# Performance work log

Hardware: AMD Instinct MI355X
Metric: run time of the kernel (lower is better)

## Reference

```python
import jax, jax.numpy as jnp
import numpy as np

FLOW_NUM = 2048
H = 64  # lstm_output_dim
NOISE_DIM = 3


def _w(key, shape, s=0.08):
    return (jax.random.normal(key, shape, dtype=jnp.float32) * s)


def setup_inputs() -> dict:
    key = jax.random.key(0)
    ks = jax.random.split(key, 20)
    d = {
        "noise": jax.random.normal(ks[0], (FLOW_NUM, NOISE_DIM), dtype=jnp.float32),
        "w_ih0": _w(ks[1], (4 * H, NOISE_DIM)),
        "w_hh0": _w(ks[2], (4 * H, H)),
        "b_ih0": _w(ks[3], (4 * H,)),
        "b_hh0": _w(ks[4], (4 * H,)),
        "w_ih1": _w(ks[5], (4 * H, H)),
        "w_hh1": _w(ks[6], (4 * H, H)),
        "b_ih1": _w(ks[7], (4 * H,)),
        "b_hh1": _w(ks[8], (4 * H,)),
        "w_ih2": _w(ks[9], (4 * H, H)),
        "w_hh2": _w(ks[10], (4 * H, H)),
        "b_ih2": _w(ks[11], (4 * H,)),
        "b_hh2": _w(ks[12], (4 * H,)),
        "fc1_w": _w(ks[13], (32, H)),
        "fc1_b": _w(ks[14], (32,)),
        "fc2_w": _w(ks[15], (16, 32)),
        "fc2_b": _w(ks[16], (16,)),
        "fc3_w": _w(ks[17], (3, 16)),
        "fc3_b": _w(ks[18], (3,)),
        "flow_length": 500,
    }
    return d


def _lstm_cell(x, h, c, w_ih, w_hh, b_ih, b_hh):
    # PyTorch gate order: input, forget, cell(g), output
    gates = x @ w_ih.T + h @ w_hh.T + (b_ih + b_hh)
    i, f, g, o = jnp.split(gates, 4, axis=-1)
    c_new = jax.nn.sigmoid(f) * c + jax.nn.sigmoid(i) * jnp.tanh(g)
    h_new = jax.nn.sigmoid(o) * jnp.tanh(c_new)
    return h_new, c_new


def reference(noise, w_ih0, w_hh0, b_ih0, b_hh0,
              w_ih1, w_hh1, b_ih1, b_hh1,
              w_ih2, w_hh2, b_ih2, b_hh2,
              fc1_w, fc1_b, fc2_w, fc2_b, fc3_w, fc3_b,
              flow_length):
    layers = [(w_ih0, w_hh0, b_ih0, b_hh0),
              (w_ih1, w_hh1, b_ih1, b_hh1),
              (w_ih2, w_hh2, b_ih2, b_hh2)]
    n = noise.shape[0]
    h0 = jnp.zeros((3, n, H), dtype=noise.dtype)
    c0 = jnp.zeros((3, n, H), dtype=noise.dtype)

    def step(carry, _):
        x, h, c = carry
        inp = x
        hs, cs = [], []
        for l, (wi, wh, bi, bh) in enumerate(layers):
            h_l, c_l = _lstm_cell(inp, h[l], c[l], wi, wh, bi, bh)
            hs.append(h_l)
            cs.append(c_l)
            inp = h_l
        # MLP head (Dropout is identity in eval mode); LeakyReLU slope 0.01
        y = jax.nn.leaky_relu(inp @ fc1_w.T + fc1_b)
        y = jax.nn.leaky_relu(y @ fc2_w.T + fc2_b)
        y = jax.nn.leaky_relu(y @ fc3_w.T + fc3_b)
        return (y, jnp.stack(hs), jnp.stack(cs)), y

    _, flow = jax.lax.scan(step, (noise, h0, c0), None, length=flow_length)
    # flow: [flow_length, flow_num, 3] -> [flow_num, flow_length, 3]
    return jnp.swapaxes(flow, 0, 1)
```

## Files before the change

### kernel.cpp

```cpp
#include <hip/hip_runtime.h>

#define NT 512

typedef _Float16 f16x8 __attribute__((ext_vector_type(8)));
typedef float    f32x4 __attribute__((ext_vector_type(4)));
typedef unsigned u32x4 __attribute__((ext_vector_type(4)));

#define MFMA(a, b, c) __builtin_amdgcn_mfma_f32_16x16x32_f16((a), (b), (c), 0, 0, 0)

#if __has_builtin(__builtin_amdgcn_exp2f)
__device__ __forceinline__ float fexp(float x) { return __builtin_amdgcn_exp2f(x * 1.4426950408889634f); }
#else
__device__ __forceinline__ float fexp(float x) { return __expf(x); }
#endif
#if __has_builtin(__builtin_amdgcn_rcpf)
__device__ __forceinline__ float frcp(float x) { return __builtin_amdgcn_rcpf(x); }
#else
__device__ __forceinline__ float frcp(float x) { return 1.0f / x; }
#endif
__device__ __forceinline__ float sigm(float x)  { return frcp(1.0f + fexp(-x)); }
__device__ __forceinline__ float tanh_(float x) { return 1.0f - 2.0f * frcp(1.0f + fexp(2.0f * x)); }
__device__ __forceinline__ float lrelu(float x) { return x > 0.0f ? x : 0.01f * x; }

__device__ __forceinline__ f16x8 ld8(const float* p) {
    const float4* q = (const float4*)p;
    float4 a = q[0], b = q[1];
    f16x8 r = { (_Float16)a.x, (_Float16)a.y, (_Float16)a.z, (_Float16)a.w,
                (_Float16)b.x, (_Float16)b.y, (_Float16)b.z, (_Float16)b.w };
    return r;
}

__device__ __forceinline__ unsigned pkh(float a, float b) {
    auto h = __builtin_amdgcn_cvt_pkrtz(a, b);
    return __builtin_bit_cast(unsigned, h);
}
__device__ __forceinline__ unsigned shflu(unsigned v, int lane) {
    return (unsigned)__shfl((int)v, lane, 64);
}

__global__ __launch_bounds__(NT, 2)
void gen_kernel(
    const float* __restrict__ noise,
    const float* __restrict__ w_ih0, const float* __restrict__ w_hh0,
    const float* __restrict__ b_ih0, const float* __restrict__ b_hh0,
    const float* __restrict__ w_ih1, const float* __restrict__ w_hh1,
    const float* __restrict__ b_ih1, const float* __restrict__ b_hh1,
    const float* __restrict__ w_ih2, const float* __restrict__ w_hh2,
    const float* __restrict__ b_ih2, const float* __restrict__ b_hh2,
    const float* __restrict__ fc1_w, const float* __restrict__ fc1_b,
    const float* __restrict__ fc2_w, const float* __restrict__ fc2_b,
    const float* __restrict__ fc3_w, const float* __restrict__ fc3_b,
    const int*   __restrict__ flow_len_p,
    float* __restrict__ out)
{
    __shared__ _Float16 sh[3][2][16 * 64] __attribute__((aligned(16)));
    __shared__ _Float16 sx [16][40] __attribute__((aligned(16)));
    __shared__ float so[2][8][16][3] __attribute__((aligned(16)));

    const int tid  = threadIdx.x;
    const int l    = tid & 63;
    const int w    = tid >> 6;
    const int ls   = l & 15;
    const int lj   = l >> 4;
    const int base = blockIdx.x * 8;
    const int T    = flow_len_p[0];

    const int gA  = ls & 3;
    const int rA0 = gA * 64 + 4 * (2 * w + 0) + (ls >> 2);
    const int rA1 = gA * 64 + 4 * (2 * w + 1) + (ls >> 2);

    f16x8 A1[2][4], A2[2][4], A0[2][3];
#pragma unroll
    for (int kc = 0; kc < 2; ++kc) {
        A1[0][kc]     = ld8(w_ih1 + rA0 * 64 + 32 * kc + 8 * lj);
        A1[1][kc]     = ld8(w_ih1 + rA1 * 64 + 32 * kc + 8 * lj);
        A1[0][2 + kc] = ld8(w_hh1 + rA0 * 64 + 32 * kc + 8 * lj);
        A1[1][2 + kc] = ld8(w_hh1 + rA1 * 64 + 32 * kc + 8 * lj);
        A2[0][kc]     = ld8(w_ih2 + rA0 * 64 + 32 * kc + 8 * lj);
        A2[1][kc]     = ld8(w_ih2 + rA1 * 64 + 32 * kc + 8 * lj);
        A2[0][2 + kc] = ld8(w_hh2 + rA0 * 64 + 32 * kc + 8 * lj);
        A2[1][2 + kc] = ld8(w_hh2 + rA1 * 64 + 32 * kc + 8 * lj);
        A0[0][kc]     = ld8(w_hh0 + rA0 * 64 + 32 * kc + 8 * lj);
        A0[1][kc]     = ld8(w_hh0 + rA1 * 64 + 32 * kc + 8 * lj);
    }
#pragma unroll
    for (int tt = 0; tt < 2; ++tt) {
        const int r = tt ? rA1 : rA0;
        f16x8 v;
#pragma unroll
        for (int i = 0; i < 8; ++i) {
            int kl = 8 * lj + i;
            float x = (kl < 3) ? w_ih0[r * 3 + kl]
                    : (kl == 3) ? (b_ih0[r] + b_hh0[r]) : 0.0f;
            v[i] = (_Float16)x;
        }
        A0[tt][2] = v;
    }
    f16x8 F1[2][2], F2, F3;
#pragma unroll
    for (int tt = 0; tt < 2; ++tt)
#pragma unroll
        for (int kc = 0; kc < 2; ++kc)
            F1[tt][kc] = ld8(fc1_w + (16 * tt + ls) * 64 + 32 * kc + 8 * lj);
    F2 = ld8(fc2_w + ls * 32 + 8 * lj);
    {
        f16x8 v;
#pragma unroll
        for (int i = 0; i < 8; ++i) {
            int k = 8 * lj + i;
            v[i] = (_Float16)((ls < 3 && k < 16) ? fc3_w[ls * 16 + k] : 0.0f);
        }
        F3 = v;
    }
    const int uc0 = 8 * w + lj, uc1 = 8 * w + 4 + lj;
    const int u_own = (ls < 8) ? uc0 : uc1;
    const int cs    = ls & 7;
    const int whaddr = cs * 64 + 8 * (((u_own >> 3) + cs) & 7) + (u_own & 7);
    float b1o[4], b2o[4];
#pragma unroll
    for (int g = 0; g < 4; ++g) {
        b1o[g] = b_ih1[g * 64 + u_own] + b_hh1[g * 64 + u_own];
        b2o[g] = b_ih2[g * 64 + u_own] + b_hh2[g * 64 + u_own];
    }
    float hb1a[4], hb1b[4], hb2[4];
#pragma unroll
    for (int r = 0; r < 4; ++r) {
        hb1a[r] = fc1_b[4 * lj + r];
        hb1b[r] = fc1_b[16 + 4 * lj + r];
        hb2[r]  = fc2_b[4 * lj + r];
    }
    float fb3[3] = { fc3_b[0], fc3_b[1], fc3_b[2] };

    const int s01 = ls + 16 * ((2 * lj) & 3);
    const int s23 = ls + 16 * ((2 * lj + 1) & 3);

    for (int i = tid; i < 3 * 2 * 16 * 64; i += NT) ((_Float16*)sh)[i] = (_Float16)0.0f;
    for (int i = tid; i < 16 * 40; i += NT) ((_Float16*)sx)[i] = (_Float16)0.0f;
    __syncthreads();
    if (tid < 16) sx[tid][3] = (_Float16)1.0f;
    if (tid < 24) {
        int s = tid / 3, d = tid % 3;
        sx[s][d] = (_Float16)noise[(base + s) * 3 + d];
    }

    float c0s = 0.0f, c1s = 0.0f, c2s = 0.0f;
    const float zb[4] = {0, 0, 0, 0};
    const f32x4 z4 = {0, 0, 0, 0};
    __syncthreads();

#define RD(L, p, kg) (*(const f16x8*)&sh[L][p][ls * 64 + 8 * (((kg) + ls) & 7)])

#define REPACK(cell, a0, a1)                                                   \
    float cell[4];                                                             \
    _Pragma("unroll")                                                          \
    for (int r = 0; r < 4; ++r) {                                              \
        float v_ = __shfl_xor(a1[r], 8);                                       \
        cell[r] = (ls < 8) ? a0[r] : v_;                                       \
    }

#define ACTC(cell, bo, cref, L, p) {                                           \
        float gi = cell[0] + bo[0], gf = cell[1] + bo[1];                      \
        float gg = cell[2] + bo[2], go = cell[3] + bo[3];                      \
        cref = sigm(gf) * cref + sigm(gi) * tanh_(gg);                         \
        sh[L][p][whaddr] = (_Float16)(sigm(go) * tanh_(cref)); }

    {
        f16x8 bx = *(const f16x8*)&sx[ls][8 * lj];
        f32x4 a0 = z4, a1 = z4;
        a0 = MFMA(A0[0][2], bx, a0);
        a1 = MFMA(A0[1][2], bx, a1);
        REPACK(cell, a0, a1)
        ACTC(cell, zb, c0s, 0, 0)
    }
    __syncthreads();
    f16x8 ph1a = RD(1, 1, lj), ph1b = RD(1, 1, 4 + lj);

    for (int t = 0; t < T; ++t) {
        const int pc = t & 1, pp = pc ^ 1;
        f16x8 r0 = RD(0, pc, lj), r1 = RD(0, pc, 4 + lj);
        f16x8 nh2a = RD(2, pp, lj), nh2b = RD(2, pp, 4 + lj);
        {
            f32x4 a0 = z4, a1 = z4;
            a0 = MFMA(A1[0][0], r0, a0);   a1 = MFMA(A1[1][0], r0, a1);
            a0 = MFMA(A1[0][1], r1, a0);   a1 = MFMA(A1[1][1], r1, a1);
            a0 = MFMA(A1[0][2], ph1a, a0); a1 = MFMA(A1[1][2], ph1a, a1);
            a0 = MFMA(A1[0][3], ph1b, a0); a1 = MFMA(A1[1][3], ph1b, a1);
            REPACK(cell, a0, a1)
            ACTC(cell, b1o, c1s, 1, pc)
        }
        __syncthreads();
        {
            f16x8 s0 = RD(1, pc, lj), s1 = RD(1, pc, 4 + lj);
            f32x4 a0 = z4, a1 = z4;
            a0 = MFMA(A2[0][0], s0, a0);   a1 = MFMA(A2[1][0], s0, a1);
            a0 = MFMA(A2[0][1], s1, a0);   a1 = MFMA(A2[1][1], s1, a1);
            a0 = MFMA(A2[0][2], nh2a, a0); a1 = MFMA(A2[1][2], nh2a, a1);
            a0 = MFMA(A2[0][3], nh2b, a0); a1 = MFMA(A2[1][3], nh2b, a1);
            REPACK(cell, a0, a1)
            ACTC(cell, b2o, c2s, 2, pc)
        }
        __syncthreads();
        f32x4 h0a = z4, h0b = z4;
        h0a = MFMA(A0[0][0], r0, h0a); h0b = MFMA(A0[1][0], r0, h0b);
        h0a = MFMA(A0[0][1], r1, h0a); h0b = MFMA(A0[1][1], r1, h0b);
        if (w == 0) {
            f16x8 bh0 = RD(2, pc, lj), bh1 = RD(2, pc, 4 + lj);
            f32x4 y1a = z4, y1b = z4;
            y1a = MFMA(F1[0][0], bh0, y1a); y1b = MFMA(F1[1][0], bh0, y1b);
            y1a = MFMA(F1[0][1], bh1, y1a); y1b = MFMA(F1[1][1], bh1, y1b);
            unsigned pa0 = pkh(lrelu(y1a[0] + hb1a[0]), lrelu(y1a[1] + hb1a[1]));
            unsigned pa1 = pkh(lrelu(y1a[2] + hb1a[2]), lrelu(y1a[3] + hb1a[3]));
            unsigned pb0 = pkh(lrelu(y1b[0] + hb1b[0]), lrelu(y1b[1] + hb1b[1]));
            unsigned pb1 = pkh(lrelu(y1b[2] + hb1b[2]), lrelu(y1b[3] + hb1b[3]));
            unsigned t0a = shflu(pa0, s01), t0b = shflu(pb0, s01);
            unsigned t1a = shflu(pa1, s01), t1b = shflu(pb1, s01);
            unsigned t2a = shflu(pa0, s23), t2b = shflu(pb0, s23);
            unsigned t3a = shflu(pa1, s23), t3b = shflu(pb1, s23);
            const bool lo = (lj < 2);
            u32x4 B1 = { lo ? t0a : t0b, lo ? t1a : t1b, lo ? t2a : t2b, lo ? t3a : t3b };
            f16x8 by1 = __builtin_bit_cast(f16x8, B1);
            f32x4 y2 = z4;
            y2 = MFMA(F2, by1, y2);
            unsigned q0 = pkh(lrelu(y2[0] + hb2[0]), lrelu(y2[1] + hb2[1]));
            unsigned q1 = pkh(lrelu(y2[2] + hb2[2]), lrelu(y2[3] + hb2[3]));
            unsigned z0 = shflu(q0, s01), z1 = shflu(q1, s01);
            unsigned z2 = shflu(q0, s23), z3 = shflu(q1, s23);
            u32x4 B2 = { z0, z1, z2, z3 };
            f16x8 by2 = __builtin_bit_cast(f16x8, B2);
            f32x4 y3 = z4;
            y3 = MFMA(F3, by2, y3);
            if (lj == 0) {
                float o0 = lrelu(y3[0] + fb3[0]);
                float o1 = lrelu(y3[1] + fb3[1]);
                float o2 = lrelu(y3[2] + fb3[2]);
                sx[ls][0] = (_Float16)o0;
                sx[ls][1] = (_Float16)o1;
                sx[ls][2] = (_Float16)o2;
                if (ls < 8) {
                    float* sp = &so[(t >> 4) & 1][ls][t & 15][0];
                    sp[0] = o0; sp[1] = o1; sp[2] = o2;
                }
            }
        }
        if (w == 7 && t >= 16 && (t & 15) == 0) {
            const int tb = t - 16, pb = (tb >> 4) & 1;
            for (int task = l; task < 96; task += 64) {
                int s = task / 12, c = task % 12;
                *(float4*)(out + ((size_t)(base + s) * T + tb) * 3 + 4 * c) =
                    *(const float4*)((const float*)&so[pb][s][0][0] + 4 * c);
            }
        }
        __syncthreads();
        {
            f16x8 bx = *(const f16x8*)&sx[ls][8 * lj];
            h0a = MFMA(A0[0][2], bx, h0a);
            h0b = MFMA(A0[1][2], bx, h0b);
            REPACK(cell, h0a, h0b)
            ACTC(cell, zb, c0s, 0, pp)
        }
        ph1a = RD(1, pc, lj); ph1b = RD(1, pc, 4 + lj);
        __syncthreads();
    }

    if (w == 7 && T > 0) {
        const int tf = ((T - 1) >> 4) << 4;
        const int pb = (tf >> 4) & 1;
        const int n  = T - tf;
        for (int task = l; task < n * 8 * 3; task += 64) {
            int s = task / (n * 3), r = task % (n * 3);
            int q = r / 3, d = r % 3;
            out[((size_t)(base + s) * T + tf + q) * 3 + d] = so[pb][s][q][d];
        }
    }
}

extern "C" void kernel_launch(void* const* d_in, const int* in_sizes, int n_in,
                              void* d_out, int out_size, void* d_ws, size_t ws_size,
                              hipStream_t stream) {
    const float* noise = (const float*)d_in[0];
    const float* w_ih0 = (const float*)d_in[1];
    const float* w_hh0 = (const float*)d_in[2];
    const float* b_ih0 = (const float*)d_in[3];
    const float* b_hh0 = (const float*)d_in[4];
    const float* w_ih1 = (const float*)d_in[5];
    const float* w_hh1 = (const float*)d_in[6];
    const float* b_ih1 = (const float*)d_in[7];
    const float* b_hh1 = (const float*)d_in[8];
    const float* w_ih2 = (const float*)d_in[9];
    const float* w_hh2 = (const float*)d_in[10];
    const float* b_ih2 = (const float*)d_in[11];
    const float* b_hh2 = (const float*)d_in[12];
    const float* fc1w  = (const float*)d_in[13];
    const float* fc1b  = (const float*)d_in[14];
    const float* fc2w  = (const float*)d_in[15];
    const float* fc2b  = (const float*)d_in[16];
    const float* fc3w  = (const float*)d_in[17];
    const float* fc3b  = (const float*)d_in[18];
    const int*   flp   = (const int*)d_in[19];

    gen_kernel<<<dim3(256), dim3(NT), 0, stream>>>(
        noise, w_ih0, w_hh0, b_ih0, b_hh0,
        w_ih1, w_hh1, b_ih1, b_hh1,
        w_ih2, w_hh2, b_ih2, b_hh2,
        fc1w, fc1b, fc2w, fc2b, fc3w, fc3b,
        flp, (float*)d_out);
}
```

Measured before the change: 822.0 us.

## Replicate MLP head in every wave and drop one barrier per timestep

Every wave now computes the small fc1/fc2/fc3 head redundantly, instead of only wave 0 computing it and broadcasting the result through shared memory. The fed-back input goes straight into the layer-0 MFMA operand in registers, which removes the sx buffer and one __syncthreads per step. The h state buffers go from double-buffered to single-buffered, and the previous h1/h2 fragments are kept in registers. In exchange, each wave does extra MFMA and shuffle work for the head on the serial critical path.

```diff
diff --git a/kernel.cpp b/kernel.cpp
--- a/kernel.cpp
+++ b/kernel.cpp
@@ -28,6 +28,13 @@
     f16x8 r = { (_Float16)a.x, (_Float16)a.y, (_Float16)a.z, (_Float16)a.w,
                 (_Float16)b.x, (_Float16)b.y, (_Float16)b.z, (_Float16)b.w };
     return r;
+}
+
+__device__ __forceinline__ f16x8 zero8() {
+    f16x8 z;
+#pragma unroll
+    for (int i = 0; i < 8; ++i) z[i] = (_Float16)0.0f;
+    return z;
 }
 
 __device__ __forceinline__ unsigned pkh(float a, float b) {
@@ -53,8 +60,7 @@
     const int*   __restrict__ flow_len_p,
     float* __restrict__ out)
 {
-    __shared__ _Float16 sh[3][2][16 * 64] __attribute__((aligned(16)));
-    __shared__ _Float16 sx [16][40] __attribute__((aligned(16)));
+    __shared__ _Float16 sh[3][16 * 64] __attribute__((aligned(16)));
     __shared__ float so[2][8][16][3] __attribute__((aligned(16)));
 
     const int tid  = threadIdx.x;
@@ -134,21 +140,14 @@
     const int s01 = ls + 16 * ((2 * lj) & 3);
     const int s23 = ls + 16 * ((2 * lj + 1) & 3);
 
-    for (int i = tid; i < 3 * 2 * 16 * 64; i += NT) ((_Float16*)sh)[i] = (_Float16)0.0f;
-    for (int i = tid; i < 16 * 40; i += NT) ((_Float16*)sx)[i] = (_Float16)0.0f;
+    for (int i = tid; i < 3 * 16 * 64; i += NT) ((_Float16*)sh)[i] = (_Float16)0.0f;
     __syncthreads();
-    if (tid < 16) sx[tid][3] = (_Float16)1.0f;
-    if (tid < 24) {
-        int s = tid / 3, d = tid % 3;
-        sx[s][d] = (_Float16)noise[(base + s) * 3 + d];
-    }
 
     float c0s = 0.0f, c1s = 0.0f, c2s = 0.0f;
     const float zb[4] = {0, 0, 0, 0};
     const f32x4 z4 = {0, 0, 0, 0};
-    __syncthreads();
-
-#define RD(L, p, kg) (*(const f16x8*)&sh[L][p][ls * 64 + 8 * (((kg) + ls) & 7)])
+
+#define RD(L, kg) (*(const f16x8*)&sh[L][ls * 64 + 8 * (((kg) + ls) & 7)])
 
 #define REPACK(cell, a0, a1)                                                   \
     float cell[4];                                                             \
@@ -158,56 +157,64 @@
         cell[r] = (ls < 8) ? a0[r] : v_;                                       \
     }
 
-#define ACTC(cell, bo, cref, L, p) {                                           \
+#define ACTC(cell, bo, cref, L) {                                              \
         float gi = cell[0] + bo[0], gf = cell[1] + bo[1];                      \
         float gg = cell[2] + bo[2], go = cell[3] + bo[3];                      \
         cref = sigm(gf) * cref + sigm(gi) * tanh_(gg);                         \
-        sh[L][p][whaddr] = (_Float16)(sigm(go) * tanh_(cref)); }
+        sh[L][whaddr] = (_Float16)(sigm(go) * tanh_(cref)); }
 
     {
-        f16x8 bx = *(const f16x8*)&sx[ls][8 * lj];
+        f16x8 bx0 = zero8();
+        if (lj == 0) {
+            float n0 = 0.0f, n1 = 0.0f, n2 = 0.0f;
+            if (ls < 8) {
+                const float* np = noise + (size_t)(base + ls) * 3;
+                n0 = np[0]; n1 = np[1]; n2 = np[2];
+            }
+            bx0[0] = (_Float16)n0; bx0[1] = (_Float16)n1;
+            bx0[2] = (_Float16)n2; bx0[3] = (_Float16)1.0f;
+        }
         f32x4 a0 = z4, a1 = z4;
-        a0 = MFMA(A0[0][2], bx, a0);
-        a1 = MFMA(A0[1][2], bx, a1);
+        a0 = MFMA(A0[0][2], bx0, a0);
+        a1 = MFMA(A0[1][2], bx0, a1);
         REPACK(cell, a0, a1)
-        ACTC(cell, zb, c0s, 0, 0)
-    }
+        ACTC(cell, zb, c0s, 0)
+    }
+    f16x8 h1r0 = zero8(), h1r1 = zero8();
+    f16x8 h2r0 = zero8(), h2r1 = zero8();
     __syncthreads();
-    f16x8 ph1a = RD(1, 1, lj), ph1b = RD(1, 1, 4 + lj);
 
     for (int t = 0; t < T; ++t) {
-        const int pc = t & 1, pp = pc ^ 1;
-        f16x8 r0 = RD(0, pc, lj), r1 = RD(0, pc, 4 + lj);
-        f16x8 nh2a = RD(2, pp, lj), nh2b = RD(2, pp, 4 + lj);
+        f16x8 r0 = RD(0, lj), r1 = RD(0, 4 + lj);
         {
             f32x4 a0 = z4, a1 = z4;
+            a0 = MFMA(A1[0][2], h1r0, a0); a1 = MFMA(A1[1][2], h1r0, a1);
+            a0 = MFMA(A1[0][3], h1r1, a0); a1 = MFMA(A1[1][3], h1r1, a1);
             a0 = MFMA(A1[0][0], r0, a0);   a1 = MFMA(A1[1][0], r0, a1);
             a0 = MFMA(A1[0][1], r1, a0);   a1 = MFMA(A1[1][1], r1, a1);
-            a0 = MFMA(A1[0][2], ph1a, a0); a1 = MFMA(A1[1][2], ph1a, a1);
-            a0 = MFMA(A1[0][3], ph1b, a0); a1 = MFMA(A1[1][3], ph1b, a1);
             REPACK(cell, a0, a1)
-            ACTC(cell, b1o, c1s, 1, pc)
+            ACTC(cell, b1o, c1s, 1)
         }
         __syncthreads();
+        h1r0 = RD(1, lj); h1r1 = RD(1, 4 + lj);
         {
-            f16x8 s0 = RD(1, pc, lj), s1 = RD(1, pc, 4 + lj);
             f32x4 a0 = z4, a1 = z4;
-            a0 = MFMA(A2[0][0], s0, a0);   a1 = MFMA(A2[1][0], s0, a1);
-            a0 = MFMA(A2[0][1], s1, a0);   a1 = MFMA(A2[1][1], s1, a1);
-            a0 = MFMA(A2[0][2], nh2a, a0); a1 = MFMA(A2[1][2], nh2a, a1);
-            a0 = MFMA(A2[0][3], nh2b, a0); a1 = MFMA(A2[1][3], nh2b, a1);
+            a0 = MFMA(A2[0][2], h2r0, a0); a1 = MFMA(A2[1][2], h2r0, a1);
+            a0 = MFMA(A2[0][3], h2r1, a0); a1 = MFMA(A2[1][3], h2r1, a1);
+            a0 = MFMA(A2[0][0], h1r0, a0); a1 = MFMA(A2[1][0], h1r0, a1);
+            a0 = MFMA(A2[0][1], h1r1, a0); a1 = MFMA(A2[1][1], h1r1, a1);
             REPACK(cell, a0, a1)
-            ACTC(cell, b2o, c2s, 2, pc)
+            ACTC(cell, b2o, c2s, 2)
         }
         __syncthreads();
-        f32x4 h0a = z4, h0b = z4;
-        h0a = MFMA(A0[0][0], r0, h0a); h0b = MFMA(A0[1][0], r0, h0b);
-        h0a = MFMA(A0[0][1], r1, h0a); h0b = MFMA(A0[1][1], r1, h0b);
-        if (w == 0) {
-            f16x8 bh0 = RD(2, pc, lj), bh1 = RD(2, pc, 4 + lj);
+        h2r0 = RD(2, lj); h2r1 = RD(2, 4 + lj);
+        {
+            f32x4 h0a = z4, h0b = z4;
+            h0a = MFMA(A0[0][0], r0, h0a); h0b = MFMA(A0[1][0], r0, h0b);
+            h0a = MFMA(A0[0][1], r1, h0a); h0b = MFMA(A0[1][1], r1, h0b);
             f32x4 y1a = z4, y1b = z4;
-            y1a = MFMA(F1[0][0], bh0, y1a); y1b = MFMA(F1[1][0], bh0, y1b);
-            y1a = MFMA(F1[0][1], bh1, y1a); y1b = MFMA(F1[1][1], bh1, y1b);
+            y1a = MFMA(F1[0][0], h2r0, y1a); y1b = MFMA(F1[1][0], h2r0, y1b);
+            y1a = MFMA(F1[0][1], h2r1, y1a); y1b = MFMA(F1[1][1], h2r1, y1b);
             unsigned pa0 = pkh(lrelu(y1a[0] + hb1a[0]), lrelu(y1a[1] + hb1a[1]));
             unsigned pa1 = pkh(lrelu(y1a[2] + hb1a[2]), lrelu(y1a[3] + hb1a[3]));
             unsigned pb0 = pkh(lrelu(y1b[0] + hb1b[0]), lrelu(y1b[1] + hb1b[1]));
@@ -229,18 +236,22 @@
             f16x8 by2 = __builtin_bit_cast(f16x8, B2);
             f32x4 y3 = z4;
             y3 = MFMA(F3, by2, y3);
+            f16x8 bx = zero8();
             if (lj == 0) {
                 float o0 = lrelu(y3[0] + fb3[0]);
                 float o1 = lrelu(y3[1] + fb3[1]);
                 float o2 = lrelu(y3[2] + fb3[2]);
-                sx[ls][0] = (_Float16)o0;
-                sx[ls][1] = (_Float16)o1;
-                sx[ls][2] = (_Float16)o2;
-                if (ls < 8) {
+                bx[0] = (_Float16)o0; bx[1] = (_Float16)o1;
+                bx[2] = (_Float16)o2; bx[3] = (_Float16)1.0f;
+                if (w == 0 && ls < 8) {
                     float* sp = &so[(t >> 4) & 1][ls][t & 15][0];
                     sp[0] = o0; sp[1] = o1; sp[2] = o2;
                 }
             }
+            h0a = MFMA(A0[0][2], bx, h0a);
+            h0b = MFMA(A0[1][2], bx, h0b);
+            REPACK(cell, h0a, h0b)
+            ACTC(cell, zb, c0s, 0)
         }
         if (w == 7 && t >= 16 && (t & 15) == 0) {
             const int tb = t - 16, pb = (tb >> 4) & 1;
@@ -250,15 +261,6 @@
                     *(const float4*)((const float*)&so[pb][s][0][0] + 4 * c);
             }
         }
-        __syncthreads();
-        {
-            f16x8 bx = *(const f16x8*)&sx[ls][8 * lj];
-            h0a = MFMA(A0[0][2], bx, h0a);
-            h0b = MFMA(A0[1][2], bx, h0b);
-            REPACK(cell, h0a, h0b)
-            ACTC(cell, zb, c0s, 0, pp)
-        }
-        ph1a = RD(1, pc, lj); ph1b = RD(1, pc, 4 + lj);
         __syncthreads();
     }
 
```

Result: no change. 813.7 us (-1.0%).
